# Kernel tuning notes

Hardware: AMD Instinct MI355X
Metric: run time of the kernel (lower is better)

The kernel has to match this reference:

```python
import jax, jax.numpy as jnp
import numpy as np


def _gcn_norm(edge_index, num_nodes):
    # PyG GCNConv default: add self-loops, symmetric normalization
    row, col = edge_index[0], edge_index[1]
    loop = jnp.arange(num_nodes, dtype=edge_index.dtype)
    row = jnp.concatenate([row, loop])
    col = jnp.concatenate([col, loop])
    deg = jax.ops.segment_sum(jnp.ones_like(col, dtype=jnp.float32), col,
                              num_segments=num_nodes)
    dinv = jnp.where(deg > 0, jax.lax.rsqrt(deg), 0.0)
    norm = dinv[row] * dinv[col]  # [E + N]
    return row, col, norm


def _gcn_conv(x, W, b, row, col, norm, num_nodes):
    h = x @ W                          # [N, H] dense transform first
    msg = h[row] * norm[:, None]       # gather + scale, [E+N, H]
    out = jax.ops.segment_sum(msg, col, num_segments=num_nodes)  # scatter-add
    return out + b


def setup_inputs() -> dict:
    key = jax.random.key(0)
    N, E, F_IN, H = 50000, 1600000, 128, 128
    ks = jax.random.split(key, 12)
    inp = {
        "x": jax.random.normal(ks[0], (N, F_IN), dtype=jnp.float32),
        "edge_index": jax.random.randint(ks[1], (2, E), 0, N, dtype=jnp.int64),
        "pos": jax.random.normal(ks[2], (N, 2), dtype=jnp.float32),
        "W1": jax.random.normal(ks[3], (F_IN, H), dtype=jnp.float32) / np.sqrt(F_IN),
        "b1": jnp.zeros((H,), dtype=jnp.float32),
        "W2": jax.random.normal(ks[4], (H, H), dtype=jnp.float32) / np.sqrt(H),
        "b2": jnp.zeros((H,), dtype=jnp.float32),
        "W3": jax.random.normal(ks[5], (H, H), dtype=jnp.float32) / np.sqrt(H),
        "b3": jnp.zeros((H,), dtype=jnp.float32),
        "Wl": jax.random.normal(ks[6], (H, 1), dtype=jnp.float32) / np.sqrt(H),
        "bl": jnp.zeros((1,), dtype=jnp.float32),
    }
    return inp


def reference(x, edge_index, pos, W1, b1, W2, b2, W3, b3, Wl, bl):
    N = x.shape[0]
    row, col, norm = _gcn_norm(edge_index, N)  # shared across the 3 convs
    h = jax.nn.relu(_gcn_conv(x, W1, b1, row, col, norm, N))
    h = jax.nn.relu(_gcn_conv(h, W2, b2, row, col, norm, N))
    h = _gcn_conv(h, W3, b3, row, col, norm, N)
    # batch = zeros -> single graph: global mean pool over all nodes -> [1, H]
    g = jnp.mean(h, axis=0, keepdims=True)
    # dropout is identity in eval mode
    out = jax.nn.sigmoid(g @ Wl + bl)  # [1, 1]
    return out
```

## Files before the change

kernel.cpp:

```cpp
#include <hip/hip_runtime.h>

#define CH 128
#define CHUNK 4096
#define SLOTS 32768
#define SCAP 12288

typedef float v2f __attribute__((ext_vector_type(2)));
typedef __attribute__((ext_vector_type(8))) short bf16x8;
typedef __attribute__((ext_vector_type(4))) float f32x4;


__device__ __forceinline__ void fp8acc4(unsigned w, v2f* a) {
  a[0] += __builtin_amdgcn_cvt_pk_f32_fp8(w, false);
  a[1] += __builtin_amdgcn_cvt_pk_f32_fp8(w, true);
}
__device__ __forceinline__ void fp8acc16(uint4 v, v2f* a) {
  fp8acc4(v.x, a); fp8acc4(v.y, a + 2); fp8acc4(v.z, a + 4); fp8acc4(v.w, a + 6);
}
__device__ __forceinline__ unsigned fp8pk4(float a, float b, float c, float d) {
  int w = 0;
  w = __builtin_amdgcn_cvt_pk_fp8_f32(a, b, w, false);
  w = __builtin_amdgcn_cvt_pk_fp8_f32(c, d, w, true);
  return (unsigned)w;
}


__device__ __forceinline__ unsigned bfpack2(float a, float b) {
  unsigned ua = __float_as_uint(a); ua += 0x7FFF + ((ua >> 16) & 1);
  unsigned ub = __float_as_uint(b); ub += 0x7FFF + ((ub >> 16) & 1);
  return (ua >> 16) | (ub & 0xFFFF0000u);
}
__device__ __forceinline__ ushort bf16of(float a) {
  unsigned ua = __float_as_uint(a); ua += 0x7FFF + ((ua >> 16) & 1);
  return (ushort)(ua >> 16);
}


__device__ __forceinline__ int edge_at(const void* ei, long long i, int is64) {
  if (is64) return (int)((const long long*)ei)[i];
  return ((const int*)ei)[i];
}

__device__ __forceinline__ int detect64(const void* ei) {
  int lane = threadIdx.x & 63;
  int v = ((const int*)ei)[2 * lane + 1];
  return (__ballot(v != 0) == 0ULL) ? 1 : 0;
}

__device__ __forceinline__ void gather_row(const uint4* __restrict__ hb,
                                           const int* __restrict__ rowptr,
                                           const int* __restrict__ src,
                                           int c, int tx, v2f* acc) {
  fp8acc16(hb[(size_t)c * 8 + tx], acc);
  int j = rowptr[c], je = rowptr[c + 1];
  for (; j < je && (j & 3); ++j) fp8acc16(hb[(size_t)src[j] * 8 + tx], acc);
  for (; j + 16 <= je; j += 16) {
    int4 s0 = *(const int4*)(src + j);
    int4 s1 = *(const int4*)(src + j + 4);
    int4 s2 = *(const int4*)(src + j + 8);
    int4 s3 = *(const int4*)(src + j + 12);
    uint4 v0 = hb[(size_t)s0.x * 8 + tx];
    uint4 v1 = hb[(size_t)s0.y * 8 + tx];
    uint4 v2 = hb[(size_t)s0.z * 8 + tx];
    uint4 v3 = hb[(size_t)s0.w * 8 + tx];
    uint4 v4 = hb[(size_t)s1.x * 8 + tx];
    uint4 v5 = hb[(size_t)s1.y * 8 + tx];
    uint4 v6 = hb[(size_t)s1.z * 8 + tx];
    uint4 v7 = hb[(size_t)s1.w * 8 + tx];
    uint4 v8 = hb[(size_t)s2.x * 8 + tx];
    uint4 v9 = hb[(size_t)s2.y * 8 + tx];
    uint4 va = hb[(size_t)s2.z * 8 + tx];
    uint4 vb = hb[(size_t)s2.w * 8 + tx];
    uint4 vc = hb[(size_t)s3.x * 8 + tx];
    uint4 vd = hb[(size_t)s3.y * 8 + tx];
    uint4 ve = hb[(size_t)s3.z * 8 + tx];
    uint4 vf = hb[(size_t)s3.w * 8 + tx];
    fp8acc16(v0, acc); fp8acc16(v1, acc); fp8acc16(v2, acc); fp8acc16(v3, acc);
    fp8acc16(v4, acc); fp8acc16(v5, acc); fp8acc16(v6, acc); fp8acc16(v7, acc);
    fp8acc16(v8, acc); fp8acc16(v9, acc); fp8acc16(va, acc); fp8acc16(vb, acc);
    fp8acc16(vc, acc); fp8acc16(vd, acc); fp8acc16(ve, acc); fp8acc16(vf, acc);
  }
  if (j + 8 <= je) {
    int4 s0 = *(const int4*)(src + j);
    int4 s1 = *(const int4*)(src + j + 4);
    uint4 v0 = hb[(size_t)s0.x * 8 + tx];
    uint4 v1 = hb[(size_t)s0.y * 8 + tx];
    uint4 v2 = hb[(size_t)s0.z * 8 + tx];
    uint4 v3 = hb[(size_t)s0.w * 8 + tx];
    uint4 v4 = hb[(size_t)s1.x * 8 + tx];
    uint4 v5 = hb[(size_t)s1.y * 8 + tx];
    uint4 v6 = hb[(size_t)s1.z * 8 + tx];
    uint4 v7 = hb[(size_t)s1.w * 8 + tx];
    fp8acc16(v0, acc); fp8acc16(v1, acc); fp8acc16(v2, acc); fp8acc16(v3, acc);
    fp8acc16(v4, acc); fp8acc16(v5, acc); fp8acc16(v6, acc); fp8acc16(v7, acc);
    j += 8;
  }
  if (j + 4 <= je) {
    int4 s0 = *(const int4*)(src + j);
    uint4 v0 = hb[(size_t)s0.x * 8 + tx];
    uint4 v1 = hb[(size_t)s0.y * 8 + tx];
    uint4 v2 = hb[(size_t)s0.z * 8 + tx];
    uint4 v3 = hb[(size_t)s0.w * 8 + tx];
    fp8acc16(v0, acc); fp8acc16(v1, acc); fp8acc16(v2, acc); fp8acc16(v3, acc);
    j += 4;
  }
  for (; j < je; ++j) fp8acc16(hb[(size_t)src[j] * 8 + tx], acc);
}

__global__ __launch_bounds__(256) void kb_scat(const void* ei,
                                               int* gcur, int* rcur,
                                               unsigned* __restrict__ cpk,
                                               unsigned* __restrict__ rpk,
                                               const float* __restrict__ W1,
                                               const float* __restrict__ b1,
                                               const float* __restrict__ W2,
                                               const float* __restrict__ b2,
                                               ushort* __restrict__ Wt1,
                                               ushort* __restrict__ Wt2,
                                               float* __restrict__ b1p,
                                               float* __restrict__ b2p,
                                               int E, int N, int nCk) {
  int t = threadIdx.x;
  if ((int)blockIdx.x >= nCk) {
    int pb = blockIdx.x - nCk;
    int base = pb * 1024;
#pragma unroll
    for (int k = 0; k < 4; ++k) {
      int i = base + k * 256 + t;
      int n = i >> 7, kk = i & 127;
      Wt1[i] = bf16of(W1[(size_t)kk * CH + n]);
      int ko = (kk & 7) * 16 + (kk >> 3);
      Wt2[i] = bf16of(W2[(size_t)ko * CH + n]);
    }
    if (pb == 0 && t < CH) b1p[t] = b1[(t & 7) * 16 + (t >> 3)];
    if (pb == 1 && t < CH) b2p[t] = b2[(t & 7) * 16 + (t >> 3)];
    return;
  }
  __shared__ int hist[256], lcur[256], gbl[256];
  int e0 = blockIdx.x * CHUNK;
  int f = detect64(ei);
  int rr[16], cc[16];
#pragma unroll
  for (int k = 0; k < 16; ++k) {
    int e = e0 + k * 256 + t;
    rr[k] = 0; cc[k] = -1;
    if (e < E) {
      int r = edge_at(ei, e, f);
      int c = edge_at(ei, (long long)E + e, f);
      if ((unsigned)r < (unsigned)N && (unsigned)c < (unsigned)N) { rr[k] = r; cc[k] = c; }
    }
  }
  hist[t] = 0;
  __syncthreads();
#pragma unroll
  for (int k = 0; k < 16; ++k)
    if (cc[k] >= 0) atomicAdd(&hist[cc[k] >> 8], 1);
  __syncthreads();
  if (hist[t] > 0) gbl[t] = atomicAdd(&gcur[t * 16], hist[t]);
  lcur[t] = 0;
  __syncthreads();
#pragma unroll
  for (int k = 0; k < 16; ++k) {
    if (cc[k] >= 0) {
      int b = cc[k] >> 8;
      int pos = gbl[b] + atomicAdd(&lcur[b], 1);
      if (pos < SLOTS)
        cpk[(size_t)b * SLOTS + pos] = (unsigned)rr[k] | ((unsigned)(cc[k] & 255) << 24);
    }
  }
  __syncthreads();
  hist[t] = 0;
  __syncthreads();
#pragma unroll
  for (int k = 0; k < 16; ++k)
    if (cc[k] >= 0) atomicAdd(&hist[rr[k] >> 8], 1);
  __syncthreads();
  if (hist[t] > 0) gbl[t] = atomicAdd(&rcur[t * 16], hist[t]);
  lcur[t] = 0;
  __syncthreads();
#pragma unroll
  for (int k = 0; k < 16; ++k) {
    if (cc[k] >= 0) {
      int b = rr[k] >> 8;
      int pos = gbl[b] + atomicAdd(&lcur[b], 1);
      if (pos < SLOTS)
        rpk[(size_t)b * SLOTS + pos] = (unsigned)cc[k] | ((unsigned)(rr[k] & 255) << 24);
    }
  }
}

__global__ __launch_bounds__(1024) void kb_csr(const unsigned* __restrict__ cpk,
                                               const int* __restrict__ gcur,
                                               int* rowptr, int* src,
                                               float* __restrict__ dinv, int N) {
  __shared__ int hist[256], lcur[256], tmp[256];
  __shared__ int baseSh;
  __shared__ int srcl[SCAP];
  int t = threadIdx.x;
  int b = blockIdx.x;
  int node0 = b << 8;
  int nn = min(256, N - node0);
  int cnt = min(gcur[b * 16], SLOTS);
  if (t < 256) tmp[t] = min(gcur[t * 16], SLOTS);
  __syncthreads();
  for (int off = 1; off < 256; off <<= 1) {
    int u = (t < 256 && t >= off) ? tmp[t - off] : 0;
    __syncthreads();
    if (t < 256) tmp[t] += u;
    __syncthreads();
  }
  if (t == 0) baseSh = tmp[b] - cnt;
  __syncthreads();
  int base = baseSh;
  if (b == (int)gridDim.x - 1 && t == 0) rowptr[N] = base + cnt;

  const unsigned* reg = cpk + (size_t)b * SLOTS;
  if (t < 256) hist[t] = 0;
  __syncthreads();
  for (int j = t; j < cnt; j += 1024)
    atomicAdd(&hist[reg[j] >> 24], 1);
  __syncthreads();
  if (t < 256) tmp[t] = hist[t];
  __syncthreads();
  for (int off = 1; off < 256; off <<= 1) {
    int u = (t < 256 && t >= off) ? tmp[t - off] : 0;
    __syncthreads();
    if (t < 256) tmp[t] += u;
    __syncthreads();
  }
  if (t < 256) {
    int v = hist[t];
    lcur[t] = tmp[t] - v;
    if (t < nn) {
      rowptr[node0 + t] = base + tmp[t] - v;
      dinv[node0 + t] = rsqrtf((float)(v + 1));
    }
  }
  __syncthreads();
  for (int j = t; j < cnt; j += 1024) {
    unsigned w = reg[j];
    int pos = atomicAdd(&lcur[w >> 24], 1);
    if (pos < SCAP) srcl[pos] = (int)(w & 0xFFFFFF);
    else            src[base + pos] = (int)(w & 0xFFFFFF);
  }
  __syncthreads();
  int m = min(cnt, SCAP);
  for (int j = t; j < m; j += 1024) src[base + j] = srcl[j];
}

__global__ __launch_bounds__(256) void k_g1wp(const float* __restrict__ Ain,
                                              const ushort* __restrict__ Wt,
                                              const float* __restrict__ dinv,
                                              uint2* __restrict__ Cb,
                                              const unsigned* __restrict__ rpk,
                                              const int* __restrict__ rcur,
                                              float* __restrict__ wp,
                                              int N, int gblocks) {
  __shared__ __align__(16) ushort smem[192 * 136];
  int t = threadIdx.x;

  if ((int)blockIdx.x >= gblocks) {
    float* wpl = (float*)smem;
    int b = blockIdx.x - gblocks;
    int node0 = b << 8;
    int nn = min(256, N - node0);
    int cnt = min(rcur[b * 16], SLOTS);
    wpl[t] = 0.f;
    __syncthreads();
    const unsigned* reg = rpk + (size_t)b * SLOTS;
    for (int j = t; j < cnt; j += 256) {
      unsigned w = reg[j];
      atomicAdd(&wpl[w >> 24], dinv[w & 0xFFFFFF]);
    }
    __syncthreads();
    if (t < nn) wp[node0 + t] = wpl[t];
    return;
  }

  ushort* As = smem;
  ushort* Bs = smem + 64 * 136;
  int row0 = blockIdx.x * 64;
  {
    const float4* A = (const float4*)Ain;
    int k4 = t & 31, m0 = t >> 5;
    for (int mm = m0; mm < 64; mm += 8) {
      int gr = row0 + mm;
      float4 v = make_float4(0.f, 0.f, 0.f, 0.f);
      if (gr < N) v = A[(size_t)gr * 32 + k4];
      *(uint2*)&As[mm * 136 + k4 * 4] = make_uint2(bfpack2(v.x, v.y), bfpack2(v.z, v.w));
    }
  }
  {
    const uint4* W4 = (const uint4*)Wt;
    int rw = t >> 1, half = t & 1;
#pragma unroll
    for (int i = 0; i < 8; ++i) {
      uint4 v = W4[rw * 16 + half * 8 + i];
      *(uint4*)&Bs[rw * 136 + half * 64 + i * 8] = v;
    }
  }
  __syncthreads();

  int lane = t & 63, w = t >> 6;
  int m = lane & 15, quad = lane >> 4;
  f32x4 acc[8] = {};
#pragma unroll
  for (int kb = 0; kb < 128; kb += 32) {
    bf16x8 af = *(const bf16x8*)&As[(w * 16 + m) * 136 + kb + quad * 8];
#pragma unroll
    for (int nt = 0; nt < 8; ++nt) {
      bf16x8 bfv = *(const bf16x8*)&Bs[(nt * 16 + m) * 136 + kb + quad * 8];
      acc[nt] = __builtin_amdgcn_mfma_f32_16x16x32_bf16(af, bfv, acc[nt], 0, 0, 0);
    }
  }
#pragma unroll
  for (int reg = 0; reg < 4; ++reg) {
    int gr = row0 + w * 16 + quad * 4 + reg;
    if (gr < N) {
      float s = dinv[gr];
      unsigned w0 = fp8pk4(acc[0][reg] * s, acc[1][reg] * s, acc[2][reg] * s, acc[3][reg] * s);
      unsigned w1 = fp8pk4(acc[4][reg] * s, acc[5][reg] * s, acc[6][reg] * s, acc[7][reg] * s);
      Cb[(size_t)gr * 16 + m] = make_uint2(w0, w1);
    }
  }
}

__global__ __launch_bounds__(256) void k_aggemm(const uint4* __restrict__ hb,
                                                const float* __restrict__ dinv,
                                                const int* __restrict__ rowptr,
                                                const int* __restrict__ src,
                                                const float* __restrict__ biasH,
                                                const ushort* __restrict__ Wt,
                                                uint2* __restrict__ Cb, int N) {
  __shared__ __align__(16) ushort As[64 * 136];
  __shared__ __align__(16) ushort Bs[128 * 136];
  int t = threadIdx.x;
  int row0 = blockIdx.x * 64;

  {
    const uint4* W4 = (const uint4*)Wt;
    int rw = t >> 1, half = t & 1;
#pragma unroll
    for (int i = 0; i < 8; ++i) {
      uint4 v = W4[rw * 16 + half * 8 + i];
      *(uint4*)&Bs[rw * 136 + half * 64 + i * 8] = v;
    }
  }

  int tx = t & 7, ty = t >> 3;
  float bv[16];
#pragma unroll
  for (int i = 0; i < 16; ++i) bv[i] = biasH[tx * 16 + i];

#pragma unroll
  for (int half = 0; half < 2; ++half) {
    int row = half * 32 + ty;
    int c = row0 + row;
    float o[16];
    if (c < N) {
      v2f acc[8] = {};
      gather_row(hb, rowptr, src, c, tx, acc);
      float s = dinv[c];
#pragma unroll
      for (int i = 0; i < 16; ++i) o[i] = fmaxf(acc[i >> 1][i & 1] * s + bv[i], 0.f);
    } else {
#pragma unroll
      for (int i = 0; i < 16; ++i) o[i] = 0.f;
    }
#pragma unroll
    for (int i = 0; i < 8; ++i)
      *(unsigned*)&As[row * 136 + tx * 16 + 2 * i] = bfpack2(o[2 * i], o[2 * i + 1]);
  }
  __syncthreads();

  int lane = t & 63, w = t >> 6;
  int m = lane & 15, quad = lane >> 4;
  f32x4 acc[8] = {};
#pragma unroll
  for (int kb = 0; kb < 128; kb += 32) {
    bf16x8 af = *(const bf16x8*)&As[(w * 16 + m) * 136 + kb + quad * 8];
#pragma unroll
    for (int nt = 0; nt < 8; ++nt) {
      bf16x8 bfv = *(const bf16x8*)&Bs[(nt * 16 + m) * 136 + kb + quad * 8];
      acc[nt] = __builtin_amdgcn_mfma_f32_16x16x32_bf16(af, bfv, acc[nt], 0, 0, 0);
    }
  }
#pragma unroll
  for (int reg = 0; reg < 4; ++reg) {
    int gr = row0 + w * 16 + quad * 4 + reg;
    if (gr < N) {
      float s = dinv[gr];
      unsigned w0 = fp8pk4(acc[0][reg] * s, acc[1][reg] * s, acc[2][reg] * s, acc[3][reg] * s);
      unsigned w1 = fp8pk4(acc[4][reg] * s, acc[5][reg] * s, acc[6][reg] * s, acc[7][reg] * s);
      Cb[(size_t)gr * 16 + m] = make_uint2(w0, w1);
    }
  }
}

__global__ __launch_bounds__(256) void k_aggfin(const uint4* __restrict__ hb,
                                                const float* __restrict__ dinv,
                                                const float* __restrict__ wp,
                                                const int* __restrict__ rowptr,
                                                const int* __restrict__ src,
                                                const float* __restrict__ biasH,
                                                float* __restrict__ part, int N) {
  int t = threadIdx.x;
  int tx = t & 7, ty = t >> 3;
  float bv[16];
#pragma unroll
  for (int i = 0; i < 16; ++i) bv[i] = biasH[tx * 16 + i];
  float wacc[16];
#pragma unroll
  for (int i = 0; i < 16; ++i) wacc[i] = 0.f;

  for (int c = blockIdx.x * 32 + ty; c < N; c += gridDim.x * 32) {
    v2f acc[8] = {};
    gather_row(hb, rowptr, src, c, tx, acc);
    float s = dinv[c];
    float wt = (s + wp[c]) * s;
#pragma unroll
    for (int i = 0; i < 16; ++i)
      wacc[i] += wt * fmaxf(acc[i >> 1][i & 1] * s + bv[i], 0.f);
  }

#pragma unroll
  for (int i = 0; i < 16; ++i) {
    wacc[i] += __shfl_down(wacc[i], 32);
    wacc[i] += __shfl_down(wacc[i], 16);
    wacc[i] += __shfl_down(wacc[i], 8);
  }
  __shared__ float redw[4][8][16];
  int wv = ty >> 3;
  if ((ty & 7) == 0) {
#pragma unroll
    for (int i = 0; i < 16; ++i) redw[wv][tx][i] = wacc[i];
  }
  __syncthreads();
  if (t < 128) {
    int cx = t >> 4, i = t & 15;
    float sum = redw[0][cx][i] + redw[1][cx][i] + redw[2][cx][i] + redw[3][cx][i];
    atomicAdd(&part[(size_t)(blockIdx.x & 63) * CH + cx * 16 + i], sum);
  }
}

__global__ __launch_bounds__(1024) void k_final(const float* __restrict__ partial,
                                                const float* __restrict__ W3,
                                                const float* __restrict__ b3,
                                                const float* __restrict__ Wl,
                                                const float* __restrict__ bl,
                                                float* __restrict__ out, float invN) {
  __shared__ float us[CH];
  __shared__ float red[8][CH];
  int t = threadIdx.x;
  int ch = t & 127, g = t >> 7;
  float s = 0.f;
#pragma unroll
  for (int b = 0; b < 8; ++b)
    s += partial[(size_t)(g * 8 + b) * CH + ch];
  red[g][ch] = s;
  __syncthreads();
  if (g == 0) {
    float u = 0.f;
#pragma unroll
    for (int k = 1; k < 8; ++k) u += red[k][ch];
    us[ch] = (s + u) * invN;
  }
  __syncthreads();
  float p = 0.f;
#pragma unroll
  for (int k = 0; k < 16; ++k) {
    int kk = g * 16 + k;
    int ko = (kk & 7) * 16 + (kk >> 3);
    p += us[kk] * W3[(size_t)ko * CH + ch];
  }
  red[g][ch] = p;
  __syncthreads();
  if (g == 0) {
    float S = red[0][ch];
#pragma unroll
    for (int k = 1; k < 8; ++k) S += red[k][ch];
    us[ch] = (S + b3[ch]) * Wl[ch];
  }
  __syncthreads();
  for (int off = 64; off > 0; off >>= 1) {
    if (t < off) us[t] += us[t + off];
    __syncthreads();
  }
  if (t == 0) out[0] = 1.f / (1.f + expf(-(us[0] + bl[0])));
}


extern "C" void kernel_launch(void* const* d_in, const int* in_sizes, int n_in,
                              void* d_out, int out_size, void* d_ws, size_t ws_size,
                              hipStream_t stream) {
  const float* x  = (const float*)d_in[0];
  const void*  ei = d_in[1];
  const float* W1 = (const float*)d_in[3];
  const float* b1 = (const float*)d_in[4];
  const float* W2 = (const float*)d_in[5];
  const float* b2 = (const float*)d_in[6];
  const float* W3 = (const float*)d_in[7];
  const float* b3 = (const float*)d_in[8];
  const float* Wl = (const float*)d_in[9];
  const float* bl = (const float*)d_in[10];
  float* out = (float*)d_out;

  const int N = in_sizes[0] / CH;
  const int E = in_sizes[1] / 2;
  const int NB = (N + 255) >> 8;

  char* ws = (char*)d_ws;
  size_t off = 0;
  auto alloc = [&](size_t bytes) -> void* {
    void* p = ws + off;
    off += (bytes + 511) & ~(size_t)511;
    return p;
  };
  float*    dinv   = (float*)alloc((size_t)N * 4);
  int*      rowptr = (int*)alloc((size_t)(N + 1) * 4);
  ushort*   Wt1    = (ushort*)alloc(128 * 128 * 2);
  ushort*   Wt2    = (ushort*)alloc(128 * 128 * 2);
  float*    b1p    = (float*)alloc(CH * 4);
  float*    b2p    = (float*)alloc(CH * 4);
  float*    wp     = (float*)alloc((size_t)N * 4);
  int*      src    = (int*)alloc((size_t)E * 4);
  unsigned* cpk    = (unsigned*)alloc((size_t)256 * SLOTS * 4);
  unsigned* rpk    = (unsigned*)alloc((size_t)256 * SLOTS * 4);
  uint4*    hb     = (uint4*)alloc((size_t)N * 128);
  uint4*    xb     = (uint4*)alloc((size_t)N * 128);
  size_t z0 = off;
  int*      gcur   = (int*)alloc(256 * 16 * 4);
  int*      rcur   = (int*)alloc(256 * 16 * 4);
  float*    part   = (float*)alloc((size_t)64 * CH * 4);
  size_t zbytes = off - z0;

  const int nCk = (E + CHUNK - 1) / CHUNK;
  const int gblocks = (N + 63) / 64;
  const int pgx = (N + 31) / 32;

  hipMemsetAsync(ws + z0, 0, zbytes, stream);
  kb_scat<<<nCk + 16, 256, 0, stream>>>(ei, gcur, rcur, cpk, rpk,
                                        W1, b1, W2, b2, Wt1, Wt2, b1p, b2p, E, N, nCk);
  kb_csr<<<NB, 1024, 0, stream>>>(cpk, gcur, rowptr, src, dinv, N);

  k_g1wp<<<gblocks + NB, 256, 0, stream>>>(x, Wt1, dinv, (uint2*)hb,
                                           rpk, rcur, wp, N, gblocks);
  k_aggemm<<<gblocks, 256, 0, stream>>>(hb, dinv, rowptr, src, b1p, Wt2, (uint2*)xb, N);
  k_aggfin<<<pgx, 256, 0, stream>>>(xb, dinv, wp, rowptr, src, b2p, part, N);
  k_final<<<1, 1024, 0, stream>>>(part, W3, b3, Wl, bl, out, 1.0f / (float)N);
}
```

Before: 235.5 us.

## Fuse first GEMM into CSR build kernel and move wp pass into aggemm

The CSR-building kernel now also runs the first dense transform (x@W1 in bf16 MFMA) for its 256-node block, using locally computed dinv from shared memory instead of a separate kernel re-reading dinv. The wp weighted-degree pass moves into extra blocks of the aggregation-GEMM kernel, which removes one launch. SCAP shrinks so the larger shared-memory footprint (A/B tiles) fits, so more edges spill straight to global memory. The 1024-thread blocks now use only 256 threads' worth of MFMA work per 16-row wave layout, and occupancy drops because of the heavy LDS use.

```diff
diff --git a/kernel.cpp b/kernel.cpp
--- a/kernel.cpp
+++ b/kernel.cpp
@@ -3,7 +3,7 @@
 #define CH 128
 #define CHUNK 4096
 #define SLOTS 32768
-#define SCAP 12288
+#define SCAP 8192
 
 typedef float v2f __attribute__((ext_vector_type(2)));
 typedef __attribute__((ext_vector_type(8))) short bf16x8;
@@ -189,13 +189,19 @@
   }
 }
 
-__global__ __launch_bounds__(1024) void kb_csr(const unsigned* __restrict__ cpk,
-                                               const int* __restrict__ gcur,
-                                               int* rowptr, int* src,
-                                               float* __restrict__ dinv, int N) {
+__global__ __launch_bounds__(1024) void kb_csrg1(const unsigned* __restrict__ cpk,
+                                                 const int* __restrict__ gcur,
+                                                 int* rowptr, int* src,
+                                                 float* __restrict__ dinv,
+                                                 const float* __restrict__ Ain,
+                                                 const ushort* __restrict__ Wt,
+                                                 uint2* __restrict__ Cb, int N) {
   __shared__ int hist[256], lcur[256], tmp[256];
+  __shared__ float dloc[256];
   __shared__ int baseSh;
   __shared__ int srcl[SCAP];
+  __shared__ __align__(16) ushort As[256 * 136];
+  __shared__ __align__(16) ushort Bs[128 * 136];
   int t = threadIdx.x;
   int b = blockIdx.x;
   int node0 = b << 8;
@@ -231,9 +237,11 @@
   if (t < 256) {
     int v = hist[t];
     lcur[t] = tmp[t] - v;
+    float dv = rsqrtf((float)(v + 1));
+    dloc[t] = dv;
     if (t < nn) {
       rowptr[node0 + t] = base + tmp[t] - v;
-      dinv[node0 + t] = rsqrtf((float)(v + 1));
+      dinv[node0 + t] = dv;
     }
   }
   __syncthreads();
@@ -244,60 +252,24 @@
     else            src[base + pos] = (int)(w & 0xFFFFFF);
   }
   __syncthreads();
-  int m = min(cnt, SCAP);
-  for (int j = t; j < m; j += 1024) src[base + j] = srcl[j];
-}
-
-__global__ __launch_bounds__(256) void k_g1wp(const float* __restrict__ Ain,
-                                              const ushort* __restrict__ Wt,
-                                              const float* __restrict__ dinv,
-                                              uint2* __restrict__ Cb,
-                                              const unsigned* __restrict__ rpk,
-                                              const int* __restrict__ rcur,
-                                              float* __restrict__ wp,
-                                              int N, int gblocks) {
-  __shared__ __align__(16) ushort smem[192 * 136];
-  int t = threadIdx.x;
-
-  if ((int)blockIdx.x >= gblocks) {
-    float* wpl = (float*)smem;
-    int b = blockIdx.x - gblocks;
-    int node0 = b << 8;
-    int nn = min(256, N - node0);
-    int cnt = min(rcur[b * 16], SLOTS);
-    wpl[t] = 0.f;
-    __syncthreads();
-    const unsigned* reg = rpk + (size_t)b * SLOTS;
-    for (int j = t; j < cnt; j += 256) {
-      unsigned w = reg[j];
-      atomicAdd(&wpl[w >> 24], dinv[w & 0xFFFFFF]);
-    }
-    __syncthreads();
-    if (t < nn) wp[node0 + t] = wpl[t];
-    return;
-  }
-
-  ushort* As = smem;
-  ushort* Bs = smem + 64 * 136;
-  int row0 = blockIdx.x * 64;
+  int mo = min(cnt, SCAP);
+  for (int j = t; j < mo; j += 1024) src[base + j] = srcl[j];
+
   {
     const float4* A = (const float4*)Ain;
     int k4 = t & 31, m0 = t >> 5;
-    for (int mm = m0; mm < 64; mm += 8) {
-      int gr = row0 + mm;
+    for (int mm = m0; mm < 256; mm += 32) {
+      int gr = node0 + mm;
       float4 v = make_float4(0.f, 0.f, 0.f, 0.f);
       if (gr < N) v = A[(size_t)gr * 32 + k4];
       *(uint2*)&As[mm * 136 + k4 * 4] = make_uint2(bfpack2(v.x, v.y), bfpack2(v.z, v.w));
     }
-  }
-  {
     const uint4* W4 = (const uint4*)Wt;
-    int rw = t >> 1, half = t & 1;
-#pragma unroll
-    for (int i = 0; i < 8; ++i) {
-      uint4 v = W4[rw * 16 + half * 8 + i];
-      *(uint4*)&Bs[rw * 136 + half * 64 + i * 8] = v;
-    }
+    int rw = t >> 3, q = t & 7;
+    uint4 v0 = W4[rw * 16 + 2 * q];
+    uint4 v1 = W4[rw * 16 + 2 * q + 1];
+    *(uint4*)&Bs[rw * 136 + q * 16] = v0;
+    *(uint4*)&Bs[rw * 136 + q * 16 + 8] = v1;
   }
   __syncthreads();
 
@@ -314,12 +286,13 @@
     }
   }
 #pragma unroll
-  for (int reg = 0; reg < 4; ++reg) {
-    int gr = row0 + w * 16 + quad * 4 + reg;
+  for (int rg = 0; rg < 4; ++rg) {
+    int lr = w * 16 + quad * 4 + rg;
+    int gr = node0 + lr;
     if (gr < N) {
-      float s = dinv[gr];
-      unsigned w0 = fp8pk4(acc[0][reg] * s, acc[1][reg] * s, acc[2][reg] * s, acc[3][reg] * s);
-      unsigned w1 = fp8pk4(acc[4][reg] * s, acc[5][reg] * s, acc[6][reg] * s, acc[7][reg] * s);
+      float s = dloc[lr];
+      unsigned w0 = fp8pk4(acc[0][rg] * s, acc[1][rg] * s, acc[2][rg] * s, acc[3][rg] * s);
+      unsigned w1 = fp8pk4(acc[4][rg] * s, acc[5][rg] * s, acc[6][rg] * s, acc[7][rg] * s);
       Cb[(size_t)gr * 16 + m] = make_uint2(w0, w1);
     }
   }
@@ -331,12 +304,34 @@
                                                 const int* __restrict__ src,
                                                 const float* __restrict__ biasH,
                                                 const ushort* __restrict__ Wt,
-                                                uint2* __restrict__ Cb, int N) {
+                                                uint2* __restrict__ Cb,
+                                                const unsigned* __restrict__ rpk,
+                                                const int* __restrict__ rcur,
+                                                float* __restrict__ wp,
+                                                int N, int gblocks) {
   __shared__ __align__(16) ushort As[64 * 136];
   __shared__ __align__(16) ushort Bs[128 * 136];
   int t = threadIdx.x;
+
+  if ((int)blockIdx.x >= gblocks) {
+    float* wpl = (float*)As;
+    int b = blockIdx.x - gblocks;
+    int node0 = b << 8;
+    int nn = min(256, N - node0);
+    int cnt = min(rcur[b * 16], SLOTS);
+    wpl[t] = 0.f;
+    __syncthreads();
+    const unsigned* reg = rpk + (size_t)b * SLOTS;
+    for (int j = t; j < cnt; j += 256) {
+      unsigned w = reg[j];
+      atomicAdd(&wpl[w >> 24], dinv[w & 0xFFFFFF]);
+    }
+    __syncthreads();
+    if (t < nn) wp[node0 + t] = wpl[t];
+    return;
+  }
+
   int row0 = blockIdx.x * 64;
-
   {
     const uint4* W4 = (const uint4*)Wt;
     int rw = t >> 1, half = t & 1;
@@ -541,11 +536,10 @@
   hipMemsetAsync(ws + z0, 0, zbytes, stream);
   kb_scat<<<nCk + 16, 256, 0, stream>>>(ei, gcur, rcur, cpk, rpk,
                                         W1, b1, W2, b2, Wt1, Wt2, b1p, b2p, E, N, nCk);
-  kb_csr<<<NB, 1024, 0, stream>>>(cpk, gcur, rowptr, src, dinv, N);
-
-  k_g1wp<<<gblocks + NB, 256, 0, stream>>>(x, Wt1, dinv, (uint2*)hb,
-                                           rpk, rcur, wp, N, gblocks);
-  k_aggemm<<<gblocks, 256, 0, stream>>>(hb, dinv, rowptr, src, b1p, Wt2, (uint2*)xb, N);
+  kb_csrg1<<<NB, 1024, 0, stream>>>(cpk, gcur, rowptr, src, dinv, x, Wt1, (uint2*)hb, N);
+
+  k_aggemm<<<gblocks + NB, 256, 0, stream>>>(hb, dinv, rowptr, src, b1p, Wt2, (uint2*)xb,
+                                             rpk, rcur, wp, N, gblocks);
   k_aggfin<<<pgx, 256, 0, stream>>>(xb, dinv, wp, rowptr, src, b2p, part, N);
   k_final<<<1, 1024, 0, stream>>>(part, W3, b3, Wl, bl, out, 1.0f / (float)N);
 }
```

After: 214.0 us. 1.1x faster.
